# Kernel optimization log

Hardware: AMD Instinct MI355X
Metric: run time of the kernel (lower is better)

The kernel has to match this reference:

```python
import jax, jax.numpy as jnp
import numpy as np

HIDDEN = 32
PAD = 2


def setup_inputs() -> dict:
    key = jax.random.key(0)
    ks = jax.random.split(key, 7)
    B, C, D, H, W = 4, 256, 32, 64, 64
    x = jax.random.normal(ks[0], (B, C, D, H, W), dtype=jnp.float32)
    # PyTorch LSTMCell params: W_ih (4H, in=1), W_hh (4H, H), biases (4H,)
    s_ih = 1.0 / np.sqrt(HIDDEN)
    W_ih = jax.random.uniform(ks[1], (4 * HIDDEN, 1), jnp.float32, -s_ih, s_ih)
    W_hh = jax.random.uniform(ks[2], (4 * HIDDEN, HIDDEN), jnp.float32, -s_ih, s_ih)
    b_ih = jax.random.uniform(ks[3], (4 * HIDDEN,), jnp.float32, -s_ih, s_ih)
    b_hh = jax.random.uniform(ks[4], (4 * HIDDEN,), jnp.float32, -s_ih, s_ih)
    gate_w = jax.random.uniform(ks[5], (1, HIDDEN), jnp.float32, -s_ih, s_ih)
    gate_b = jax.random.uniform(ks[6], (1,), jnp.float32, -s_ih, s_ih)
    return {"x": x, "W_ih": W_ih, "W_hh": W_hh, "b_ih": b_ih, "b_hh": b_hh,
            "gate_w": gate_w, "gate_b": gate_b}


def reference(x, W_ih, W_hh, b_ih, b_hh, gate_w, gate_b):
    B, C, D, H, W = x.shape
    p = PAD
    # ReflectionPad3d on spatial dims
    xp = jnp.pad(x, ((0, 0), (0, 0), (p, p), (p, p), (p, p)), mode="reflect")
    # per-channel spatial mean over the PADDED volume -> (B, C)
    channel_seq = xp.reshape(B, C, -1).mean(axis=2)
    bias = b_ih + b_hh  # (4H,)

    def step(carry, inp_t):  # inp_t: (B,) scalar channel feature per batch
        h, c = carry
        # gates: (B, 4H); input_size=1 so W_ih contributes inp * W_ih[:,0]
        z = inp_t[:, None] * W_ih[:, 0][None, :] + h @ W_hh.T + bias
        i, f, g, o = jnp.split(z, 4, axis=1)  # PyTorch i,f,g,o ordering
        c = jax.nn.sigmoid(f) * c + jax.nn.sigmoid(i) * jnp.tanh(g)
        h = jax.nn.sigmoid(o) * jnp.tanh(c)
        return (h, c), h

    h0 = jnp.zeros((B, HIDDEN), x.dtype)
    c0 = jnp.zeros((B, HIDDEN), x.dtype)
    _, hs = jax.lax.scan(step, (h0, c0), channel_seq.T)  # hs: (C, B, H)
    seq_outputs = hs.transpose(1, 0, 2)  # (B, C, H)
    # AlphaDropout is identity in eval mode
    gates = jax.nn.sigmoid(seq_outputs @ gate_w[0] + gate_b[0])  # (B, C)
    # reweight padded map then crop == reweight original x (reflect-pad crop is exact)
    return x * gates[:, :, None, None, None]
```

## Files before the change

kernel.cpp:

```cpp
#include <hip/hip_runtime.h>


#define CH_F4 32768
#define NCH 1024
#define MEAN_DEN (1.0f / 166464.0f)

typedef unsigned int uint;
typedef float f32x4 __attribute__((ext_vector_type(4)));

__device__ __forceinline__ float sigf(float x) {
    return 1.0f / (1.0f + __expf(-x));
}
__device__ __forceinline__ float tanh_fast(float x) {
    return fmaf(2.0f, sigf(2.0f * x), -1.0f);
}

__global__ __launch_bounds__(256) void mean_kernel(const float* __restrict__ x,
                                                   float* __restrict__ cseq) {
    const int bc = blockIdx.x;
    const f32x4* __restrict__ p = (const f32x4*)x + (size_t)bc * CH_F4;
    const int tid = threadIdx.x;

    float sum = 0.0f;
    for (int i = tid; i < CH_F4; i += 256) {
        f32x4 v = p[i];
        const int q = i & 15;
        const int h = (i >> 4) & 63;
        const int d = i >> 10;
        float t = (v.x + v.y) + (v.z + v.w);
        if (q == 0 || q == 15) t += v.y + v.z;
        const float wd = ((d == 1) | (d == 2) | (d == 29) | (d == 30)) ? 2.0f : 1.0f;
        const float wh = ((h == 1) | (h == 2) | (h == 61) | (h == 62)) ? 2.0f : 1.0f;
        sum = fmaf(wd * wh, t, sum);
    }

    __shared__ float red[256];
    red[tid] = sum;
    __syncthreads();
    for (int s = 128; s > 0; s >>= 1) {
        if (tid < s) red[tid] += red[tid + s];
        __syncthreads();
    }
    if (tid == 0) cseq[bc] = red[0] * MEAN_DEN;
}

__global__ __launch_bounds__(64) void lstm_kernel(const float* __restrict__ cseq,
                                                  const float* __restrict__ W_ih,
                                                  const float* __restrict__ W_hh,
                                                  const float* __restrict__ b_ih,
                                                  const float* __restrict__ b_hh,
                                                  const float* __restrict__ gate_w,
                                                  const float* __restrict__ gate_b,
                                                  float* __restrict__ gates) {
    __shared__ float cs[256];
    __shared__ float hist[257 * 33];

    const int b = blockIdx.x;
    const int l = threadIdx.x;
    const int r0 = l, r1 = l + 64;

    const float wih0 = W_ih[r0];
    const float wih1 = W_ih[r1];
    const float bias0 = b_ih[r0] + b_hh[r0];
    const float bias1 = b_ih[r1] + b_hh[r1];
    float whh0[32], whh1[32];
#pragma unroll
    for (int k = 0; k < 32; k++) {
        whh0[k] = W_hh[r0 * 32 + k];
        whh1[k] = W_hh[r1 * 32 + k];
    }
#pragma unroll
    for (int i = 0; i < 4; i++) cs[i * 64 + l] = cseq[b * 256 + i * 64 + l];
    float h = 0.0f;
    float c = 0.0f;
    __syncthreads();

    for (int t = 0; t < 256; t++) {
        const float inp = cs[t];
        float z0 = fmaf(inp, wih0, bias0);
        float z1 = fmaf(inp, wih1, bias1);
#pragma unroll
        for (int k = 0; k < 32; k++) {
            const float hk = __builtin_bit_cast(float,
                __builtin_amdgcn_readlane(__builtin_bit_cast(int, h), k));
            z0 = fmaf(hk, whh0[k], z0);
            z1 = fmaf(hk, whh1[k], z1);
        }
        float zf, zo;
#if __has_builtin(__builtin_amdgcn_permlane32_swap)
        {
            auto ra = __builtin_amdgcn_permlane32_swap(
                __builtin_bit_cast(uint, z0), __builtin_bit_cast(uint, z0), false, false);
            auto rb = __builtin_amdgcn_permlane32_swap(
                __builtin_bit_cast(uint, z1), __builtin_bit_cast(uint, z1), false, false);
            zf = __builtin_bit_cast(float, ra[1]);
            zo = __builtin_bit_cast(float, rb[1]);
        }
#else
        zf = __shfl_xor(z0, 32);
        zo = __shfl_xor(z1, 32);
#endif
        c = sigf(zf) * c + sigf(z0) * tanh_fast(z1);
        h = sigf(zo) * tanh_fast(c);
        if (l < 32) hist[(t + 1) * 33 + l] = h;
    }
    __syncthreads();

    float gw[32];
#pragma unroll
    for (int k = 0; k < 32; k++) gw[k] = gate_w[k];
    const float gb = gate_b[0];
#pragma unroll
    for (int chunk = 0; chunk < 4; chunk++) {
        const int t = chunk * 64 + l;
        const float* hrow = &hist[(t + 1) * 33];
        float s = gb;
#pragma unroll
        for (int k = 0; k < 32; k++) s = fmaf(hrow[k], gw[k], s);
        gates[b * 256 + t] = sigf(s);
    }
}

__global__ __launch_bounds__(256) void scale_kernel(const float* __restrict__ x,
                                                    const float* __restrict__ gates,
                                                    float* __restrict__ out) {
    const int bc = (NCH - 1) - blockIdx.y;
    const float g = gates[bc];
    const size_t base = (size_t)bc * CH_F4;
    const f32x4* __restrict__ xi = (const f32x4*)x + base;
    f32x4* __restrict__ oi = (f32x4*)out + base;
    const int start = blockIdx.x * 1024 + threadIdx.x;
#pragma unroll
    for (int r = 0; r < 4; r++) {
        const int idx = start + r * 256;
        f32x4 v = xi[idx];
        v *= g;
        __builtin_nontemporal_store(v, &oi[idx]);
    }
}

extern "C" void kernel_launch(void* const* d_in, const int* in_sizes, int n_in,
                              void* d_out, int out_size, void* d_ws, size_t ws_size,
                              hipStream_t stream) {
    const float* x      = (const float*)d_in[0];
    const float* W_ih   = (const float*)d_in[1];
    const float* W_hh   = (const float*)d_in[2];
    const float* b_ih   = (const float*)d_in[3];
    const float* b_hh   = (const float*)d_in[4];
    const float* gate_w = (const float*)d_in[5];
    const float* gate_b = (const float*)d_in[6];
    float* out = (float*)d_out;

    float* cseq  = (float*)d_ws;
    float* gates = (float*)d_ws + 1024;

    mean_kernel<<<NCH, 256, 0, stream>>>(x, cseq);
    lstm_kernel<<<4, 64, 0, stream>>>(cseq, W_ih, W_hh, b_ih, b_hh,
                                      gate_w, gate_b, gates);
    scale_kernel<<<dim3(32, NCH), 256, 0, stream>>>(x, gates, out);
}
```

Baseline: 406.1 us.

## Fuse mean, LSTM and scale into one cooperative kernel with grid syncs

Replaces the three separate launches with a single cooperative kernel of 512 blocks. Each block reduces two channels, all blocks grid-sync, four blocks run the LSTM, they grid-sync again, and then each block scales its two channels. This removes launch gaps and may let the scale pass reuse channel data still in cache, but the whole grid idles during the serial LSTM phase and the scale phase now runs with far fewer blocks. If the cooperative launch fails, it falls back to three launches of the same kernel.

```diff
diff --git a/kernel.cpp b/kernel.cpp
--- a/kernel.cpp
+++ b/kernel.cpp
@@ -1,8 +1,11 @@
 #include <hip/hip_runtime.h>
+#include <hip/hip_cooperative_groups.h>
+
+namespace cg = cooperative_groups;
 
 
 #define CH_F4 32768
-#define NCH 1024
+#define GRID 512
 #define MEAN_DEN (1.0f / 166464.0f)
 
 typedef unsigned int uint;
@@ -15,127 +18,139 @@
     return fmaf(2.0f, sigf(2.0f * x), -1.0f);
 }
 
-__global__ __launch_bounds__(256) void mean_kernel(const float* __restrict__ x,
-                                                   float* __restrict__ cseq) {
-    const int bc = blockIdx.x;
-    const f32x4* __restrict__ p = (const f32x4*)x + (size_t)bc * CH_F4;
+__global__ __launch_bounds__(256) void fused_kernel(
+    const float* __restrict__ x,
+    const float* __restrict__ W_ih, const float* __restrict__ W_hh,
+    const float* __restrict__ b_ih, const float* __restrict__ b_hh,
+    const float* __restrict__ gate_w, const float* __restrict__ gate_b,
+    float* __restrict__ out, float* __restrict__ ws, int phase_mask)
+{
+    float* __restrict__ cseq  = ws;
+    float* __restrict__ gates = ws + 1024;
+
+    __shared__ float red[256];
+    __shared__ float hist[257 * 33];
+
+    const int bc  = blockIdx.x;
     const int tid = threadIdx.x;
 
-    float sum = 0.0f;
-    for (int i = tid; i < CH_F4; i += 256) {
-        f32x4 v = p[i];
-        const int q = i & 15;
-        const int h = (i >> 4) & 63;
-        const int d = i >> 10;
-        float t = (v.x + v.y) + (v.z + v.w);
-        if (q == 0 || q == 15) t += v.y + v.z;
-        const float wd = ((d == 1) | (d == 2) | (d == 29) | (d == 30)) ? 2.0f : 1.0f;
-        const float wh = ((h == 1) | (h == 2) | (h == 61) | (h == 62)) ? 2.0f : 1.0f;
-        sum = fmaf(wd * wh, t, sum);
-    }
-
-    __shared__ float red[256];
-    red[tid] = sum;
-    __syncthreads();
-    for (int s = 128; s > 0; s >>= 1) {
-        if (tid < s) red[tid] += red[tid + s];
+    if (phase_mask & 1) {
+        const f32x4* __restrict__ p0 = (const f32x4*)x + (size_t)bc * CH_F4;
+        const f32x4* __restrict__ p1 = p0 + (size_t)GRID * CH_F4;
+        float s0 = 0.0f, s1 = 0.0f;
+        for (int i = tid; i < CH_F4; i += 256) {
+            f32x4 v0 = p0[i];
+            f32x4 v1 = p1[i];
+            const int q = i & 15;
+            const int h = (i >> 4) & 63;
+            const int d = i >> 10;
+            const float wd = ((d == 1) | (d == 2) | (d == 29) | (d == 30)) ? 2.0f : 1.0f;
+            const float wh = ((h == 1) | (h == 2) | (h == 61) | (h == 62)) ? 2.0f : 1.0f;
+            const float w = wd * wh;
+            float t0 = (v0.x + v0.y) + (v0.z + v0.w);
+            float t1 = (v1.x + v1.y) + (v1.z + v1.w);
+            if (q == 0 || q == 15) {
+                t0 += v0.y + v0.z;
+                t1 += v1.y + v1.z;
+            }
+            s0 = fmaf(w, t0, s0);
+            s1 = fmaf(w, t1, s1);
+        }
+        red[tid] = s0;
+        __syncthreads();
+        for (int s = 128; s > 0; s >>= 1) {
+            if (tid < s) red[tid] += red[tid + s];
+            __syncthreads();
+        }
+        if (tid == 0) cseq[bc] = red[0] * MEAN_DEN;
+        __syncthreads();
+        red[tid] = s1;
+        __syncthreads();
+        for (int s = 128; s > 0; s >>= 1) {
+            if (tid < s) red[tid] += red[tid + s];
+            __syncthreads();
+        }
+        if (tid == 0) cseq[bc + GRID] = red[0] * MEAN_DEN;
         __syncthreads();
     }
-    if (tid == 0) cseq[bc] = red[0] * MEAN_DEN;
-}
+    if (phase_mask == 7) cg::this_grid().sync();
 
-__global__ __launch_bounds__(64) void lstm_kernel(const float* __restrict__ cseq,
-                                                  const float* __restrict__ W_ih,
-                                                  const float* __restrict__ W_hh,
-                                                  const float* __restrict__ b_ih,
-                                                  const float* __restrict__ b_hh,
-                                                  const float* __restrict__ gate_w,
-                                                  const float* __restrict__ gate_b,
-                                                  float* __restrict__ gates) {
-    __shared__ float cs[256];
-    __shared__ float hist[257 * 33];
+    if ((phase_mask & 2) && bc < 4 && tid < 64) {
+        const int b = bc, l = tid;
+        float* cs = red;
 
-    const int b = blockIdx.x;
-    const int l = threadIdx.x;
-    const int r0 = l, r1 = l + 64;
-
-    const float wih0 = W_ih[r0];
-    const float wih1 = W_ih[r1];
-    const float bias0 = b_ih[r0] + b_hh[r0];
-    const float bias1 = b_ih[r1] + b_hh[r1];
-    float whh0[32], whh1[32];
-#pragma unroll
-    for (int k = 0; k < 32; k++) {
-        whh0[k] = W_hh[r0 * 32 + k];
-        whh1[k] = W_hh[r1 * 32 + k];
-    }
-#pragma unroll
-    for (int i = 0; i < 4; i++) cs[i * 64 + l] = cseq[b * 256 + i * 64 + l];
-    float h = 0.0f;
-    float c = 0.0f;
-    __syncthreads();
-
-    for (int t = 0; t < 256; t++) {
-        const float inp = cs[t];
-        float z0 = fmaf(inp, wih0, bias0);
-        float z1 = fmaf(inp, wih1, bias1);
+        const float wih0 = W_ih[l];
+        const float wih1 = W_ih[l + 64];
+        const float bias0 = b_ih[l] + b_hh[l];
+        const float bias1 = b_ih[l + 64] + b_hh[l + 64];
+        float whh0[32], whh1[32];
 #pragma unroll
         for (int k = 0; k < 32; k++) {
-            const float hk = __builtin_bit_cast(float,
-                __builtin_amdgcn_readlane(__builtin_bit_cast(int, h), k));
-            z0 = fmaf(hk, whh0[k], z0);
-            z1 = fmaf(hk, whh1[k], z1);
+            whh0[k] = W_hh[l * 32 + k];
+            whh1[k] = W_hh[(l + 64) * 32 + k];
         }
-        float zf, zo;
+#pragma unroll
+        for (int i = 0; i < 4; i++) cs[i * 64 + l] = cseq[b * 256 + i * 64 + l];
+        float h = 0.0f, c = 0.0f;
+
+        for (int t = 0; t < 256; t++) {
+            const float inp = cs[t];
+            float z0 = fmaf(inp, wih0, bias0);
+            float z1 = fmaf(inp, wih1, bias1);
+#pragma unroll
+            for (int k = 0; k < 32; k++) {
+                const float hk = __builtin_bit_cast(float,
+                    __builtin_amdgcn_readlane(__builtin_bit_cast(int, h), k));
+                z0 = fmaf(hk, whh0[k], z0);
+                z1 = fmaf(hk, whh1[k], z1);
+            }
+            float zf, zo;
 #if __has_builtin(__builtin_amdgcn_permlane32_swap)
-        {
-            auto ra = __builtin_amdgcn_permlane32_swap(
-                __builtin_bit_cast(uint, z0), __builtin_bit_cast(uint, z0), false, false);
-            auto rb = __builtin_amdgcn_permlane32_swap(
-                __builtin_bit_cast(uint, z1), __builtin_bit_cast(uint, z1), false, false);
-            zf = __builtin_bit_cast(float, ra[1]);
-            zo = __builtin_bit_cast(float, rb[1]);
+            {
+                auto ra = __builtin_amdgcn_permlane32_swap(
+                    __builtin_bit_cast(uint, z0), __builtin_bit_cast(uint, z0), false, false);
+                auto rb = __builtin_amdgcn_permlane32_swap(
+                    __builtin_bit_cast(uint, z1), __builtin_bit_cast(uint, z1), false, false);
+                zf = __builtin_bit_cast(float, ra[1]);
+                zo = __builtin_bit_cast(float, rb[1]);
+            }
+#else
+            zf = __shfl_xor(z0, 32);
+            zo = __shfl_xor(z1, 32);
+#endif
+            c = sigf(zf) * c + sigf(z0) * tanh_fast(z1);
+            h = sigf(zo) * tanh_fast(c);
+            if (l < 32) hist[(t + 1) * 33 + l] = h;
         }
-#else
-        zf = __shfl_xor(z0, 32);
-        zo = __shfl_xor(z1, 32);
-#endif
-        c = sigf(zf) * c + sigf(z0) * tanh_fast(z1);
-        h = sigf(zo) * tanh_fast(c);
-        if (l < 32) hist[(t + 1) * 33 + l] = h;
+
+        const float gb = gate_b[0];
+#pragma unroll
+        for (int chunk = 0; chunk < 4; chunk++) {
+            const int t = chunk * 64 + l;
+            const float* hrow = &hist[(t + 1) * 33];
+            float s = gb;
+#pragma unroll
+            for (int k = 0; k < 32; k++) s = fmaf(hrow[k], gate_w[k], s);
+            gates[b * 256 + t] = sigf(s);
+        }
     }
-    __syncthreads();
+    if (phase_mask == 7) cg::this_grid().sync();
 
-    float gw[32];
-#pragma unroll
-    for (int k = 0; k < 32; k++) gw[k] = gate_w[k];
-    const float gb = gate_b[0];
-#pragma unroll
-    for (int chunk = 0; chunk < 4; chunk++) {
-        const int t = chunk * 64 + l;
-        const float* hrow = &hist[(t + 1) * 33];
-        float s = gb;
-#pragma unroll
-        for (int k = 0; k < 32; k++) s = fmaf(hrow[k], gw[k], s);
-        gates[b * 256 + t] = sigf(s);
-    }
-}
-
-__global__ __launch_bounds__(256) void scale_kernel(const float* __restrict__ x,
-                                                    const float* __restrict__ gates,
-                                                    float* __restrict__ out) {
-    const int bc = (NCH - 1) - blockIdx.y;
-    const float g = gates[bc];
-    const size_t base = (size_t)bc * CH_F4;
-    const f32x4* __restrict__ xi = (const f32x4*)x + base;
-    f32x4* __restrict__ oi = (f32x4*)out + base;
-    const int start = blockIdx.x * 1024 + threadIdx.x;
-#pragma unroll
-    for (int r = 0; r < 4; r++) {
-        const int idx = start + r * 256;
-        f32x4 v = xi[idx];
-        v *= g;
-        __builtin_nontemporal_store(v, &oi[idx]);
+    if (phase_mask & 4) {
+        const float g0 = gates[bc];
+        const float g1 = gates[bc + GRID];
+        const f32x4* __restrict__ xi0 = (const f32x4*)x + (size_t)bc * CH_F4;
+        const f32x4* __restrict__ xi1 = xi0 + (size_t)GRID * CH_F4;
+        f32x4* __restrict__ oi0 = (f32x4*)out + (size_t)bc * CH_F4;
+        f32x4* __restrict__ oi1 = oi0 + (size_t)GRID * CH_F4;
+        for (int i = tid; i < CH_F4; i += 256) {
+            f32x4 v0 = xi0[i];
+            f32x4 v1 = xi1[i];
+            v0 *= g0;
+            v1 *= g1;
+            __builtin_nontemporal_store(v0, &oi0[i]);
+            __builtin_nontemporal_store(v1, &oi1[i]);
+        }
     }
 }
 
@@ -150,12 +165,21 @@
     const float* gate_w = (const float*)d_in[5];
     const float* gate_b = (const float*)d_in[6];
     float* out = (float*)d_out;
+    float* ws  = (float*)d_ws;
 
-    float* cseq  = (float*)d_ws;
-    float* gates = (float*)d_ws + 1024;
-
-    mean_kernel<<<NCH, 256, 0, stream>>>(x, cseq);
-    lstm_kernel<<<4, 64, 0, stream>>>(cseq, W_ih, W_hh, b_ih, b_hh,
-                                      gate_w, gate_b, gates);
-    scale_kernel<<<dim3(32, NCH), 256, 0, stream>>>(x, gates, out);
+    int mask_all = 7;
+    void* args[] = {(void*)&x, (void*)&W_ih, (void*)&W_hh, (void*)&b_ih,
+                    (void*)&b_hh, (void*)&gate_w, (void*)&gate_b,
+                    (void*)&out, (void*)&ws, (void*)&mask_all};
+    hipError_t err = hipLaunchCooperativeKernel((void*)fused_kernel,
+                                                dim3(GRID), dim3(256),
+                                                args, 0, stream);
+    if (err != hipSuccess) {
+        fused_kernel<<<GRID, 256, 0, stream>>>(x, W_ih, W_hh, b_ih, b_hh,
+                                               gate_w, gate_b, out, ws, 1);
+        fused_kernel<<<4, 256, 0, stream>>>(x, W_ih, W_hh, b_ih, b_hh,
+                                            gate_w, gate_b, out, ws, 2);
+        fused_kernel<<<GRID, 256, 0, stream>>>(x, W_ih, W_hh, b_ih, b_hh,
+                                               gate_w, gate_b, out, ws, 4);
+    }
 }
```

Measured after the change: 511.2 us. 25.9% more time.

## Split channel reduction and scaling into half-channel blocks, fold partial sums in LSTM

Applied to the files above, without the earlier changes.

The mean kernel now uses two blocks per channel and writes raw partial sums. The LSTM kernel adds the two halves and applies the mean scale when it loads the sequence. The scale kernel goes from 32K small blocks to 2048 blocks, each striding over half a channel in reverse order. The LSTM also drops its __syncthreads, since the block is a single 64-lane wavefront, and its weights are now explicit scalars via macros. This trades per-block launch overhead against fewer resident waves and less latency hiding in the bandwidth-bound passes.

```diff
diff --git a/kernel.cpp b/kernel.cpp
--- a/kernel.cpp
+++ b/kernel.cpp
@@ -1,12 +1,11 @@
 #include <hip/hip_runtime.h>
 
 
-#define CH_F4 32768
-#define NCH 1024
 #define MEAN_DEN (1.0f / 166464.0f)
 
 typedef unsigned int uint;
 typedef float f32x4 __attribute__((ext_vector_type(4)));
+typedef float f32x2 __attribute__((ext_vector_type(2)));
 
 __device__ __forceinline__ float sigf(float x) {
     return 1.0f / (1.0f + __expf(-x));
@@ -16,21 +15,25 @@
 }
 
 __global__ __launch_bounds__(256) void mean_kernel(const float* __restrict__ x,
-                                                   float* __restrict__ cseq) {
-    const int bc = blockIdx.x;
-    const f32x4* __restrict__ p = (const f32x4*)x + (size_t)bc * CH_F4;
+                                                   float* __restrict__ part) {
+    const int bid = blockIdx.x;
+    const int ch = bid >> 1, half = bid & 1;
+    const f32x4* __restrict__ p = (const f32x4*)x + (size_t)ch * 32768 + half * 16384;
+    const int base = half * 16384;
     const int tid = threadIdx.x;
 
     float sum = 0.0f;
-    for (int i = tid; i < CH_F4; i += 256) {
-        f32x4 v = p[i];
+#pragma unroll 4
+    for (int il = tid; il < 16384; il += 256) {
+        f32x4 v = p[il];
+        const int i = base + il;
         const int q = i & 15;
-        const int h = (i >> 4) & 63;
+        const int hh = (i >> 4) & 63;
         const int d = i >> 10;
         float t = (v.x + v.y) + (v.z + v.w);
         if (q == 0 || q == 15) t += v.y + v.z;
         const float wd = ((d == 1) | (d == 2) | (d == 29) | (d == 30)) ? 2.0f : 1.0f;
-        const float wh = ((h == 1) | (h == 2) | (h == 61) | (h == 62)) ? 2.0f : 1.0f;
+        const float wh = ((hh == 1) | (hh == 2) | (hh == 61) | (hh == 62)) ? 2.0f : 1.0f;
         sum = fmaf(wd * wh, t, sum);
     }
 
@@ -41,17 +44,23 @@
         if (tid < s) red[tid] += red[tid + s];
         __syncthreads();
     }
-    if (tid == 0) cseq[bc] = red[0] * MEAN_DEN;
+    if (tid == 0) part[bid] = red[0];
 }
 
-__global__ __launch_bounds__(64) void lstm_kernel(const float* __restrict__ cseq,
-                                                  const float* __restrict__ W_ih,
-                                                  const float* __restrict__ W_hh,
-                                                  const float* __restrict__ b_ih,
-                                                  const float* __restrict__ b_hh,
-                                                  const float* __restrict__ gate_w,
-                                                  const float* __restrict__ gate_b,
-                                                  float* __restrict__ gates) {
+#define RL(v, k) __builtin_bit_cast(float, \
+    __builtin_amdgcn_readlane(__builtin_bit_cast(int, (v)), (k)))
+#define DW(k) const float w0_##k = W_hh[r0 * 32 + (k)]; \
+              const float w1_##k = W_hh[r1 * 32 + (k)];
+#define GK(k) { const float hk = RL(h, k); \
+                z0 = fmaf(hk, w0_##k, z0); z1 = fmaf(hk, w1_##k, z1); }
+
+__global__ __launch_bounds__(64, 1) void lstm_kernel(
+    const float* __restrict__ part,
+    const float* __restrict__ W_ih, const float* __restrict__ W_hh,
+    const float* __restrict__ b_ih, const float* __restrict__ b_hh,
+    const float* __restrict__ gate_w, const float* __restrict__ gate_b,
+    float* __restrict__ gates)
+{
     __shared__ float cs[256];
     __shared__ float hist[257 * 33];
 
@@ -63,29 +72,28 @@
     const float wih1 = W_ih[r1];
     const float bias0 = b_ih[r0] + b_hh[r0];
     const float bias1 = b_ih[r1] + b_hh[r1];
-    float whh0[32], whh1[32];
+    DW(0)  DW(1)  DW(2)  DW(3)  DW(4)  DW(5)  DW(6)  DW(7)
+    DW(8)  DW(9)  DW(10) DW(11) DW(12) DW(13) DW(14) DW(15)
+    DW(16) DW(17) DW(18) DW(19) DW(20) DW(21) DW(22) DW(23)
+    DW(24) DW(25) DW(26) DW(27) DW(28) DW(29) DW(30) DW(31)
+
+    const f32x2* __restrict__ p2 = (const f32x2*)part + b * 256;
 #pragma unroll
-    for (int k = 0; k < 32; k++) {
-        whh0[k] = W_hh[r0 * 32 + k];
-        whh1[k] = W_hh[r1 * 32 + k];
+    for (int j = 0; j < 4; j++) {
+        const int cch = j * 64 + l;
+        f32x2 pr = p2[cch];
+        cs[cch] = (pr.x + pr.y) * MEAN_DEN;
     }
-#pragma unroll
-    for (int i = 0; i < 4; i++) cs[i * 64 + l] = cseq[b * 256 + i * 64 + l];
-    float h = 0.0f;
-    float c = 0.0f;
-    __syncthreads();
 
+    float h = 0.0f, cstate = 0.0f;
     for (int t = 0; t < 256; t++) {
         const float inp = cs[t];
         float z0 = fmaf(inp, wih0, bias0);
         float z1 = fmaf(inp, wih1, bias1);
-#pragma unroll
-        for (int k = 0; k < 32; k++) {
-            const float hk = __builtin_bit_cast(float,
-                __builtin_amdgcn_readlane(__builtin_bit_cast(int, h), k));
-            z0 = fmaf(hk, whh0[k], z0);
-            z1 = fmaf(hk, whh1[k], z1);
-        }
+        GK(0)  GK(1)  GK(2)  GK(3)  GK(4)  GK(5)  GK(6)  GK(7)
+        GK(8)  GK(9)  GK(10) GK(11) GK(12) GK(13) GK(14) GK(15)
+        GK(16) GK(17) GK(18) GK(19) GK(20) GK(21) GK(22) GK(23)
+        GK(24) GK(25) GK(26) GK(27) GK(28) GK(29) GK(30) GK(31)
         float zf, zo;
 #if __has_builtin(__builtin_amdgcn_permlane32_swap)
         {
@@ -100,15 +108,11 @@
         zf = __shfl_xor(z0, 32);
         zo = __shfl_xor(z1, 32);
 #endif
-        c = sigf(zf) * c + sigf(z0) * tanh_fast(z1);
-        h = sigf(zo) * tanh_fast(c);
+        cstate = sigf(zf) * cstate + sigf(z0) * tanh_fast(z1);
+        h = sigf(zo) * tanh_fast(cstate);
         if (l < 32) hist[(t + 1) * 33 + l] = h;
     }
-    __syncthreads();
 
-    float gw[32];
-#pragma unroll
-    for (int k = 0; k < 32; k++) gw[k] = gate_w[k];
     const float gb = gate_b[0];
 #pragma unroll
     for (int chunk = 0; chunk < 4; chunk++) {
@@ -116,7 +120,7 @@
         const float* hrow = &hist[(t + 1) * 33];
         float s = gb;
 #pragma unroll
-        for (int k = 0; k < 32; k++) s = fmaf(hrow[k], gw[k], s);
+        for (int k = 0; k < 32; k++) s = fmaf(hrow[k], gate_w[k], s);
         gates[b * 256 + t] = sigf(s);
     }
 }
@@ -124,18 +128,17 @@
 __global__ __launch_bounds__(256) void scale_kernel(const float* __restrict__ x,
                                                     const float* __restrict__ gates,
                                                     float* __restrict__ out) {
-    const int bc = (NCH - 1) - blockIdx.y;
-    const float g = gates[bc];
-    const size_t base = (size_t)bc * CH_F4;
-    const f32x4* __restrict__ xi = (const f32x4*)x + base;
-    f32x4* __restrict__ oi = (f32x4*)out + base;
-    const int start = blockIdx.x * 1024 + threadIdx.x;
-#pragma unroll
-    for (int r = 0; r < 4; r++) {
-        const int idx = start + r * 256;
-        f32x4 v = xi[idx];
+    const int rb = 2047 - (int)blockIdx.x;
+    const int ch = rb >> 1, half = rb & 1;
+    const float g = gates[ch];
+    const size_t off = (size_t)ch * 32768 + half * 16384;
+    const f32x4* __restrict__ xi = (const f32x4*)x + off;
+    f32x4* __restrict__ oi = (f32x4*)out + off;
+#pragma unroll 4
+    for (int i = threadIdx.x; i < 16384; i += 256) {
+        f32x4 v = xi[i];
         v *= g;
-        __builtin_nontemporal_store(v, &oi[idx]);
+        __builtin_nontemporal_store(v, &oi[i]);
     }
 }
 
@@ -151,11 +154,11 @@
     const float* gate_b = (const float*)d_in[6];
     float* out = (float*)d_out;
 
-    float* cseq  = (float*)d_ws;
-    float* gates = (float*)d_ws + 1024;
+    float* part  = (float*)d_ws;
+    float* gates = (float*)d_ws + 2048;
 
-    mean_kernel<<<NCH, 256, 0, stream>>>(x, cseq);
-    lstm_kernel<<<4, 64, 0, stream>>>(cseq, W_ih, W_hh, b_ih, b_hh,
+    mean_kernel<<<2048, 256, 0, stream>>>(x, part);
+    lstm_kernel<<<4, 64, 0, stream>>>(part, W_ih, W_hh, b_ih, b_hh,
                                       gate_w, gate_b, gates);
-    scale_kernel<<<dim3(32, NCH), 256, 0, stream>>>(x, gates, out);
+    scale_kernel<<<2048, 256, 0, stream>>>(x, gates, out);
 }
```

Measured after the change: 409.3 us. No clear change (+0.8%).
